# Optimization experiments

Hardware: AMD Instinct MI355X
Metric: run time of the kernel (lower is better)

## Reference

```python
import jax, jax.numpy as jnp
import numpy as np

B, T, V, E, H = 64, 512, 8192, 1024, 2048


def setup_inputs() -> dict:
    key = jax.random.key(0)
    k = jax.random.split(key, 8)
    idx = jax.random.randint(k[0], (B, T), 0, V)
    targets = jax.random.randint(k[1], (B, T), 0, V)
    s = 0.02
    W_E = jax.random.normal(k[2], (V, E), jnp.float32) * s
    start = jnp.zeros((1, H), jnp.float32)
    W_xh = jax.random.normal(k[3], (E + H, H), jnp.float32) * s  # Linear(E+H -> H)
    b_xh = jnp.zeros((H,), jnp.float32)
    W_head = jax.random.normal(k[4], (H, V), jnp.float32) * s
    b_head = jnp.zeros((V,), jnp.float32)
    return {"idx": idx, "targets": targets, "W_E": W_E, "start": start,
            "W_xh": W_xh, "b_xh": b_xh, "W_head": W_head, "b_head": b_head}


def reference(idx, targets, W_E, start, W_xh, b_xh, W_head, b_head):
    b, t = idx.shape
    emb = W_E[idx]  # [B, T, E]
    # split concat-linear: cat([x,h]) @ W_xh == x @ Wx + h @ Wh (same math)
    Wx, Wh = W_xh[:E], W_xh[E:]
    xproj = jnp.einsum('bte,eh->bth', emb, Wx) + b_xh  # precompute input part

    def step(h_prev, xp_t):
        h_t = jnp.tanh(xp_t + h_prev @ Wh)
        return h_t, h_t

    h0 = jnp.broadcast_to(start, (b, H))
    _, hs = jax.lax.scan(step, h0, jnp.swapaxes(xproj, 0, 1))  # [T, B, H]
    hidden = jnp.swapaxes(hs, 0, 1)  # [B, T, H]
    logits = jnp.einsum('bth,hv->btv', hidden, W_head) + b_head

    # cross entropy with ignore_index=-1
    logp = jax.nn.log_softmax(logits, axis=-1)
    mask = targets != -1
    tsafe = jnp.where(mask, targets, 0)
    nll = -jnp.take_along_axis(logp, tsafe[..., None], axis=-1)[..., 0]
    loss = jnp.sum(nll * mask) / jnp.maximum(jnp.sum(mask), 1)
    return logits, loss
```

## Files before the change

kernel.cpp:

```cpp
#include <hip/hip_runtime.h>
#include <hip/hip_bf16.h>
#include <math.h>
#include <stdint.h>

#define Bb 64
#define Tt 512
#define Vv 8192
#define Ee 1024
#define Hh 2048

typedef unsigned short u16;
typedef unsigned long long u64;
typedef __attribute__((ext_vector_type(8))) short bf16x8;
typedef __attribute__((ext_vector_type(8))) _Float16 f16x8;
typedef __attribute__((ext_vector_type(4))) float f32x4;

__device__ __forceinline__ u16 f2b(float f) {
  unsigned u = __float_as_uint(f);
  u += 0x7FFF + ((u >> 16) & 1);
  return (u16)(u >> 16);
}
__device__ __forceinline__ float b2f(u16 h) {
  return __uint_as_float(((unsigned)h) << 16);
}
__device__ __forceinline__ u16 f2h_bits(float f) {
  union { _Float16 h; u16 u; } c;
  c.h = (_Float16)f;
  return c.u;
}

__device__ __forceinline__ void gload16f(f16x8& dst, const void* addr) {
  asm volatile("global_load_dwordx4 %0, %1, off sc1"
               : "=v"(dst) : "v"(addr) : "memory");
}
__device__ __forceinline__ void gstore2_sc1(void* addr, unsigned val) {
  asm volatile("global_store_short %0, %1, off sc1"
               :: "v"(addr), "v"(val) : "memory");
}

__device__ __forceinline__ void gll16(const u16* g, const u16* l) {
  __builtin_amdgcn_global_load_lds((__attribute__((address_space(1))) void*)g,
                                   (__attribute__((address_space(3))) void*)l, 16, 0, 0);
}

__device__ __forceinline__ float wave_max(float v) {
  #pragma unroll
  for (int d = 32; d; d >>= 1) v = fmaxf(v, __shfl_xor(v, d, 64));
  return v;
}
__device__ __forceinline__ float wave_sum(float v) {
  #pragma unroll
  for (int d = 32; d; d >>= 1) v += __shfl_xor(v, d, 64);
  return v;
}


__device__ __forceinline__ void tr_cast_f16(const float* __restrict__ src,
                                            u16* __restrict__ dst, int R, int C,
                                            int bi, int bj, int tid,
                                            float (*tile)[33]) {
  const int r  = tid >> 3;
  const int c4 = (tid & 7) * 4;
  float4 v = *(const float4*)(src + (size_t)(bj * 32 + r) * C + bi * 32 + c4);
  tile[r][c4 + 0] = v.x; tile[r][c4 + 1] = v.y;
  tile[r][c4 + 2] = v.z; tile[r][c4 + 3] = v.w;
  __syncthreads();
  ushort4 o;
  o.x = f2h_bits(tile[c4 + 0][r]); o.y = f2h_bits(tile[c4 + 1][r]);
  o.z = f2h_bits(tile[c4 + 2][r]); o.w = f2h_bits(tile[c4 + 3][r]);
  *(ushort4*)(dst + (size_t)(bi * 32 + r) * R + bj * 32 + c4) = o;
}

__global__ __launch_bounds__(256)
void prep_all(const float* __restrict__ WE, const int* __restrict__ idx,
              u16* __restrict__ emb,
              const float* __restrict__ W_xh, u16* __restrict__ WxT16,
              u16* __restrict__ WhT,
              const float* __restrict__ W_head, u16* __restrict__ WheadT,
              const float* __restrict__ start, u16* __restrict__ hbuf,
              unsigned* __restrict__ sync) {
  __shared__ float tile[32][33];
  const int b = blockIdx.x;
  const int tid = threadIdx.x;
  if (b < 32768) {
    const int row = idx[b];
    const float4 v = ((const float4*)(WE + (size_t)row * Ee))[tid];
    ushort4 o;
    o.x = f2h_bits(v.x); o.y = f2h_bits(v.y);
    o.z = f2h_bits(v.z); o.w = f2h_bits(v.w);
    ((ushort4*)(emb + (size_t)b * Ee))[tid] = o;
  } else if (b < 34816) {
    const int s = b - 32768;
    tr_cast_f16(W_xh, WxT16, Ee, Hh, s % 64, s / 64, tid, tile);
  } else if (b < 38912) {
    const int s = b - 34816;
    tr_cast_f16(W_xh + (size_t)Ee * Hh, WhT, Hh, Hh, s % 64, s / 64, tid, tile);
  } else if (b < 55296) {
    const int s = b - 38912;
    tr_cast_f16(W_head, WheadT, Hh, Vv, s % 256, s / 256, tid, tile);
  } else {
    const int s = b - 55296;
    #pragma unroll
    for (int j = 0; j < 8; ++j) {
      int n = tid * 8 + j;
      hbuf[(size_t)s * 2048 + n] = f2h_bits(start[n]);
    }
    if (s == 0) sync[tid] = 0;
  }
}

template <int MODE, int F16>
__global__ __launch_bounds__(512, 2)
void gemm256(const u16* __restrict__ A, const u16* __restrict__ Bt,
             const float* __restrict__ bias, void* __restrict__ outp,
             float* __restrict__ pm, float* __restrict__ ps,
             int M, int N, int K) {
  __shared__ u16 lds[81920];

  const int tid = threadIdx.x;
  const int lane = tid & 63;
  const int w = tid >> 6;
  const int wm = w >> 2;
  const int wn = w & 3;
  const int l15 = lane & 15, l16 = lane >> 4;

  const int nwg = gridDim.x * gridDim.y;
  const int lin = blockIdx.y * gridDim.x + blockIdx.x;
  const int swz = (lin & 7) * (nwg >> 3) + (lin >> 3);
  const int bm = swz % gridDim.x;
  const int bn = swz / gridDim.x;
  const int bm256 = bm * 256, bn256 = bn * 256;

  const size_t srcLane = (size_t)l15 * K + l16 * 8;
  #define STG(P, R0, kt, base)                                                 \
    {                                                                          \
      gll16((P) + (size_t)((R0) + w * 16) * K + (size_t)(kt) * 32 + srcLane,   \
            &lds[(base) + w * 512]);                                           \
      gll16((P) + (size_t)((R0) + (8 + w) * 16) * K + (size_t)(kt) * 32 + srcLane, \
            &lds[(base) + (8 + w) * 512]);                                     \
    }
  #define ABUF(t) (((t) % 5) * 8192)
  #define BBUF(t) (40960 + ((t) % 5) * 8192)
  #define DSF(base, rbase) \
    (*(const bf16x8*)&lds[(base) + ((rbase) >> 4) * 512 + l16 * 128 + l15 * 8])
  #define MM1(a, b, c)                                                          \
    (F16 ? __builtin_amdgcn_mfma_f32_16x16x32_f16(*(const f16x8*)&(a),          \
                                                  *(const f16x8*)&(b), (c), 0, 0, 0) \
         : __builtin_amdgcn_mfma_f32_16x16x32_bf16((a), (b), (c), 0, 0, 0))

  f32x4 acc[8][4];
  #pragma unroll
  for (int m = 0; m < 8; ++m)
    #pragma unroll
    for (int n = 0; n < 4; ++n)
      acc[m][n] = (f32x4){0.f, 0.f, 0.f, 0.f};

  const int NT = K >> 5;

  for (int pt = 0; pt < 4; ++pt) {
    STG(A,  bm256, pt, ABUF(pt));
    STG(Bt, bn256, pt, BBUF(pt));
  }
  asm volatile("s_waitcnt vmcnt(0)" ::: "memory");
  __builtin_amdgcn_s_barrier();

  for (int t = 0; t < NT; ++t) {
    const int abase = ABUF(t);
    const int bbase = BBUF(t);
    const bool stg = (t + 4 < NT);
    bf16x8 aR[8], bR[4];

    #pragma unroll
    for (int j = 0; j < 4; ++j) bR[j] = DSF(bbase, wn * 64 + j * 16);
    #pragma unroll
    for (int i = 0; i < 8; ++i) aR[i] = DSF(abase, wm * 128 + i * 16);
    if (stg) {
      STG(A,  bm256, t + 4, ABUF(t + 4));
      STG(Bt, bn256, t + 4, BBUF(t + 4));
      asm volatile("s_waitcnt vmcnt(12)" ::: "memory");
    } else {
      asm volatile("s_waitcnt vmcnt(0)" ::: "memory");
    }
    __builtin_amdgcn_s_barrier();
    asm volatile("s_waitcnt lgkmcnt(0)" ::: "memory");
    __builtin_amdgcn_sched_barrier(0);
    __builtin_amdgcn_s_setprio(1);
    #pragma unroll
    for (int i = 0; i < 8; ++i)
      #pragma unroll
      for (int j = 0; j < 4; ++j)
        acc[i][j] = MM1(aR[i], bR[j], acc[i][j]);
    __builtin_amdgcn_s_setprio(0);
    __builtin_amdgcn_s_barrier();
  }

  const int c0 = bn256 + wn * 64 + l15;
  float bv[4];
  #pragma unroll
  for (int j = 0; j < 4; ++j) bv[j] = bias[c0 + j * 16];

  if (MODE == 0) {
    float* scr = (float*)lds;
    float* outf = (float*)outp;
    #pragma unroll
    for (int fm = 0; fm < 8; ++fm) {
      #pragma unroll
      for (int q = 0; q < 4; ++q) {
        const int rl = wm * 128 + (fm >> 2) * 64 + (fm & 3) * 16 + l16 * 4 + q;
        const int row = bm256 + rl;
        float v0 = acc[fm][0][q] + bv[0];
        float v1 = acc[fm][1][q] + bv[1];
        float v2 = acc[fm][2][q] + bv[2];
        float v3 = acc[fm][3][q] + bv[3];
        outf[(size_t)row * N + c0]      = v0;
        outf[(size_t)row * N + c0 + 16] = v1;
        outf[(size_t)row * N + c0 + 32] = v2;
        outf[(size_t)row * N + c0 + 48] = v3;
        float mx = fmaxf(fmaxf(v0, v1), fmaxf(v2, v3));
        #pragma unroll
        for (int d = 1; d < 16; d <<= 1) mx = fmaxf(mx, __shfl_xor(mx, d, 64));
        float se = expf(v0 - mx) + expf(v1 - mx) + expf(v2 - mx) + expf(v3 - mx);
        #pragma unroll
        for (int d = 1; d < 16; d <<= 1) se += __shfl_xor(se, d, 64);
        if (l15 == 0) {
          scr[wn * 256 + rl] = mx;
          scr[1024 + wn * 256 + rl] = se;
        }
      }
    }
    __syncthreads();
    if (lane < 32) {
      const int rl = w * 32 + lane;
      float m0 = scr[rl], m1 = scr[256 + rl], m2 = scr[512 + rl], m3 = scr[768 + rl];
      float Mx = fmaxf(fmaxf(m0, m1), fmaxf(m2, m3));
      float S = scr[1024 + rl] * expf(m0 - Mx) + scr[1280 + rl] * expf(m1 - Mx)
              + scr[1536 + rl] * expf(m2 - Mx) + scr[1792 + rl] * expf(m3 - Mx);
      const int row = bm256 + rl;
      const int nbn = N >> 8;
      pm[(size_t)row * nbn + bn] = Mx;
      ps[(size_t)row * nbn + bn] = S;
    }
  } else {
    u16* outh = (u16*)outp;
    #pragma unroll
    for (int fm = 0; fm < 8; ++fm) {
      #pragma unroll
      for (int q = 0; q < 4; ++q) {
        const int row = bm256 + wm * 128 + (fm >> 2) * 64 + (fm & 3) * 16 + l16 * 4 + q;
        const int b = row >> 9, t = row & 511;
        u16* dst = outh + ((size_t)t * Bb + b) * N + c0;
        dst[0]  = f2b(acc[fm][0][q] + bv[0]);
        dst[16] = f2b(acc[fm][1][q] + bv[1]);
        dst[32] = f2b(acc[fm][2][q] + bv[2]);
        dst[48] = f2b(acc[fm][3][q] + bv[3]);
      }
    }
  }
  #undef STG
  #undef ABUF
  #undef BBUF
  #undef DSF
  #undef MM1
}

__global__ __launch_bounds__(512, 2)
void rnn_scan(const u16* __restrict__ WhT, const u16* __restrict__ xp,
              u16* __restrict__ hbuf, u16* __restrict__ hidden,
              unsigned* __restrict__ sync) {
  __shared__ u16 whi[65536];
  __shared__ float red[4096];

  const int bid = blockIdx.x;
  const int g = bid >> 6;
  const int colg = bid & 63;
  const int rowbase = g * 16;
  const int col0 = colg * 32;
  const int tid = threadIdx.x;
  const int lane = tid & 63;
  const int w = tid >> 6;

  for (int i = tid; i < 8192; i += 512) {
    const int ch = i & 3;
    const int cl = (i >> 2) & 15;
    const int kt = (i >> 6) & 63;
    const int c2 = (i >> 12) & 1;
    bf16x8 v = *(const bf16x8*)(WhT + (size_t)(col0 + c2 * 16 + cl) * 2048 + kt * 32 + ch * 8);
    *(bf16x8*)&whi[(size_t)(c2 * 64 + kt) * 512 + ch * 128 + cl * 8] = v;
  }
  __syncthreads();

  unsigned* cnt = sync + g * 64;
  bool dead = false;
  const int hrow = rowbase + (lane & 15);

  const int ev = w * 64 + lane;
  const int ef = ev >> 8;
  const int ep = ev & 255;
  const int el = ep >> 2, eq = ep & 3;
  const int erow = rowbase + (el & 15);
  const int ecol = col0 + ef * 16 + ((el >> 4) << 2) + eq;

  u16 xv16 = xp[(size_t)erow * 2048 + ecol];

  for (int t = 0; t < Tt; ++t) {
    const u16* hp = hbuf + (size_t)(t & 1) * (64 * 2048);
    u16*       hn = hbuf + (size_t)((t + 1) & 1) * (64 * 2048);

    f16x8 qh[8];
    const u16* hb = hp + (size_t)hrow * 2048 + (lane >> 4) * 8;
    #pragma unroll
    for (int kt = 0; kt < 8; ++kt)
      gload16f(qh[kt], hb + (w * 8 + kt) * 32);
    asm volatile("s_waitcnt vmcnt(0)" ::: "memory");
    __builtin_amdgcn_sched_barrier(0);

    f32x4 a0 = (f32x4){0.f, 0.f, 0.f, 0.f};
    f32x4 a1 = (f32x4){0.f, 0.f, 0.f, 0.f};
    #pragma unroll
    for (int kt = 0; kt < 8; ++kt) {
      const int ktG = w * 8 + kt;
      f16x8 w0 = *(const f16x8*)&whi[(size_t)(0 * 64 + ktG) * 512 + (lane >> 4) * 128 + (lane & 15) * 8];
      f16x8 w1 = *(const f16x8*)&whi[(size_t)(1 * 64 + ktG) * 512 + (lane >> 4) * 128 + (lane & 15) * 8];
      a0 = __builtin_amdgcn_mfma_f32_16x16x32_f16(w0, qh[kt], a0, 0, 0, 0);
      a1 = __builtin_amdgcn_mfma_f32_16x16x32_f16(w1, qh[kt], a1, 0, 0, 0);
    }

    *(f32x4*)&red[(w) * 256 + lane * 4]     = a0;
    *(f32x4*)&red[(8 + w) * 256 + lane * 4] = a1;
    __syncthreads();

    {
      float s = 0.f;
      #pragma unroll
      for (int j = 0; j < 8; ++j)
        s += red[(ef * 8 + j) * 256 + ep];
      float hv = tanhf(s + b2f(xv16));
      u16 hf = f2h_bits(hv);
      gstore2_sc1(hn + (size_t)erow * 2048 + ecol, (unsigned)hf);
      hidden[((size_t)erow * Tt + t) * Hh + ecol] = hf;
    }

    __syncthreads();
    if (t + 1 < Tt)
      xv16 = xp[((size_t)(t + 1) * Bb + erow) * 2048 + ecol];
    if (tid == 0) {
      unsigned old = __hip_atomic_fetch_add(cnt, 1u, __ATOMIC_RELAXED, __HIP_MEMORY_SCOPE_AGENT);
      if (old != (unsigned)(t * 64 + 63) && !dead) {
        unsigned polls = 0;
        while (__hip_atomic_load(cnt, __ATOMIC_RELAXED, __HIP_MEMORY_SCOPE_AGENT)
               < (unsigned)((t + 1) * 64)) {
          __builtin_amdgcn_s_sleep(1);
          if (++polls > 1000000u) { dead = true; break; }
        }
      }
    }
    __syncthreads();
  }
}


__global__ __launch_bounds__(256)
void nll_from_partials(const float* __restrict__ pm, const float* __restrict__ ps,
                       const float* __restrict__ logits, const int* __restrict__ tgt,
                       float* __restrict__ nll) {
  const int r = blockIdx.x * 4 + (threadIdx.x >> 6);
  const int lane = threadIdx.x & 63;
  float m = (lane < 32) ? pm[(size_t)r * 32 + lane] : -1e30f;
  float s = (lane < 32) ? ps[(size_t)r * 32 + lane] : 0.f;
  float M = wave_max(m);
  float S = wave_sum(s * expf(m - M));
  if (lane == 0) {
    const int tg = tgt[r];
    float o = 0.f;
    if (tg != -1) o = M + logf(S) - logits[(size_t)r * Vv + tg];
    nll[r] = o;
  }
}

__global__ __launch_bounds__(256)
void loss_reduce(const float* __restrict__ nll, const int* __restrict__ tgt,
                 float* __restrict__ out) {
  const int tid = threadIdx.x;
  float s = 0.f, c = 0.f;
  for (int i = tid; i < Bb * Tt; i += 256) {
    s += nll[i];
    c += (tgt[i] != -1) ? 1.f : 0.f;
  }
  s = wave_sum(s);
  c = wave_sum(c);
  __shared__ float as_[4], ac_[4];
  const int w = tid >> 6;
  if ((tid & 63) == 0) { as_[w] = s; ac_[w] = c; }
  __syncthreads();
  if (tid == 0) {
    float S = as_[0] + as_[1] + as_[2] + as_[3];
    float C = ac_[0] + ac_[1] + ac_[2] + ac_[3];
    out[0] = S / fmaxf(C, 1.f);
  }
}


extern "C" void kernel_launch(void* const* d_in, const int* in_sizes, int n_in,
                              void* d_out, int out_size, void* d_ws, size_t ws_size,
                              hipStream_t stream) {
  const int*   idx    = (const int*)d_in[0];
  const int*   tgt    = (const int*)d_in[1];
  const float* W_E    = (const float*)d_in[2];
  const float* start  = (const float*)d_in[3];
  const float* W_xh   = (const float*)d_in[4];
  const float* b_xh   = (const float*)d_in[5];
  const float* W_head = (const float*)d_in[6];
  const float* b_head = (const float*)d_in[7];

  char* ws = (char*)d_ws;
  u16*      emb16  = (u16*)(ws);
  u16*      hidden = (u16*)(ws);
  u16*      xproj  = (u16*)(ws + (size_t)128 * 1024 * 1024);
  float*    pm     = (float*)(ws + (size_t)128 * 1024 * 1024);
  float*    ps     = (float*)(ws + (size_t)136 * 1024 * 1024);
  u16*      WheadT = (u16*)(ws + (size_t)256 * 1024 * 1024);
  u16*      WhT    = (u16*)(ws + (size_t)288 * 1024 * 1024);
  u16*      WxT16  = (u16*)(ws + (size_t)304 * 1024 * 1024);
  u16*      hbuf   = (u16*)(ws + (size_t)312 * 1024 * 1024);
  float*    nll    = (float*)(ws + (size_t)313 * 1024 * 1024);
  unsigned* sync   = (unsigned*)(ws + (size_t)313 * 1024 * 1024 + 128 * 1024);

  prep_all<<<55360, 256, 0, stream>>>(W_E, idx, emb16, W_xh, WxT16, WhT,
                                      W_head, WheadT, start, hbuf, sync);

  gemm256<1, 1><<<dim3(128, 8), 512, 0, stream>>>(emb16, WxT16, b_xh, xproj, nullptr, nullptr,
                                                  Bb * Tt, Hh, 1024);

  rnn_scan<<<256, 512, 0, stream>>>(WhT, xproj, hbuf, hidden, sync);

  gemm256<0, 1><<<dim3(128, 32), 512, 0, stream>>>(hidden, WheadT, b_head, d_out, pm, ps,
                                                   Bb * Tt, Vv, 2048);

  nll_from_partials<<<Bb * Tt / 4, 256, 0, stream>>>(pm, ps, (const float*)d_out, tgt, nll);
  loss_reduce<<<1, 256, 0, stream>>>(nll, tgt, (float*)d_out + ((size_t)out_size - 1));
}
```

Baseline: 4.226 ms.

## Replace atomic counter barrier with per-block flags and master-broadcast barrier

Replaces the per-group atomic fetch-add counter barrier in the recurrent kernel with per-block flag stores on separate cache lines. One master block (colg==0) polls all 64 flags with a single wave and then publishes a generation word that the other blocks poll. This is meant to remove contention from 64 blocks doing atomic RMW and polling the same address each timestep. The cost is an extra hop of latency through the master block, and the sync buffer layout grows, so the init code now zeroes a larger region.

Result: slower. 4.366 ms (+3.3%).

```diff
diff --git a/kernel.cpp b/kernel.cpp
--- a/kernel.cpp
+++ b/kernel.cpp
@@ -105,7 +105,8 @@
       int n = tid * 8 + j;
       hbuf[(size_t)s * 2048 + n] = f2h_bits(start[n]);
     }
-    if (s == 0) sync[tid] = 0;
+    for (int i = tid; i < 320; i += 256)
+      sync[s * 320 + i] = 0;
   }
 }
 
@@ -289,7 +290,8 @@
   }
   __syncthreads();
 
-  unsigned* cnt = sync + g * 64;
+  unsigned* flags = sync + g * 5120;
+  unsigned* gn    = sync + g * 5120 + 4096;
   bool dead = false;
   const int hrow = rowbase + (lane & 15);
 
@@ -343,15 +345,30 @@
     __syncthreads();
     if (t + 1 < Tt)
       xv16 = xp[((size_t)(t + 1) * Bb + erow) * 2048 + ecol];
-    if (tid == 0) {
-      unsigned old = __hip_atomic_fetch_add(cnt, 1u, __ATOMIC_RELAXED, __HIP_MEMORY_SCOPE_AGENT);
-      if (old != (unsigned)(t * 64 + 63) && !dead) {
+    if (tid == 0)
+      __hip_atomic_store(flags + colg * 64, (unsigned)(t + 1),
+                         __ATOMIC_RELAXED, __HIP_MEMORY_SCOPE_AGENT);
+    if (colg == 0) {
+      if (w == 0 && !dead) {
+        const unsigned* fp = flags + lane * 64;
         unsigned polls = 0;
-        while (__hip_atomic_load(cnt, __ATOMIC_RELAXED, __HIP_MEMORY_SCOPE_AGENT)
-               < (unsigned)((t + 1) * 64)) {
+        for (;;) {
+          int ok = (__hip_atomic_load(fp, __ATOMIC_RELAXED, __HIP_MEMORY_SCOPE_AGENT)
+                    >= (unsigned)(t + 1));
+          if (__all(ok)) break;
           __builtin_amdgcn_s_sleep(1);
-          if (++polls > 1000000u) { dead = true; break; }
+          if (++polls > 500000u) { dead = true; break; }
         }
+        if (lane == 0)
+          __hip_atomic_store(gn, (unsigned)(t + 1),
+                             __ATOMIC_RELAXED, __HIP_MEMORY_SCOPE_AGENT);
+      }
+    } else if (tid == 0 && !dead) {
+      unsigned polls = 0;
+      while (__hip_atomic_load(gn, __ATOMIC_RELAXED, __HIP_MEMORY_SCOPE_AGENT)
+             < (unsigned)(t + 1)) {
+        __builtin_amdgcn_s_sleep(1);
+        if (++polls > 1000000u) { dead = true; break; }
       }
     }
     __syncthreads();
```
